# Kernel optimization log

Hardware: AMD Instinct MI355X
Metric: run time of the kernel (lower is better)

Reference implementation:

```python
import jax, jax.numpy as jnp
import numpy as np

NEG_SLOPE = 0.2  # PyG GATConv default


def add_self_loops(edge_index, num_nodes):
    loops = jnp.arange(num_nodes, dtype=edge_index.dtype)
    return jnp.concatenate([edge_index, jnp.stack([loops, loops])], axis=1)


def gat_conv(x, edge_index, W, att_src, att_dst, bias, heads, out_ch, concat):
    # x: [N, F_in]; edge_index: [2, E] with row0=src(j), row1=dst(i)
    N = x.shape[0]
    xl = (x @ W).reshape(N, heads, out_ch)              # [N, H, C]
    src, dst = edge_index[0], edge_index[1]
    a_src = jnp.einsum('nhc,hc->nh', xl, att_src)        # [N, H]
    a_dst = jnp.einsum('nhc,hc->nh', xl, att_dst)        # [N, H]
    alpha = jax.nn.leaky_relu(a_src[src] + a_dst[dst], NEG_SLOPE)  # [E, H]
    # segment softmax over incoming edges of each dst node
    m = jax.ops.segment_max(alpha, dst, num_segments=N)  # [N, H]
    e = jnp.exp(alpha - m[dst])
    denom = jax.ops.segment_sum(e, dst, num_segments=N)
    coef = e / (denom[dst] + 1e-16)                      # [E, H]
    msg = xl[src] * coef[..., None]                      # [E, H, C]
    out = jax.ops.segment_sum(msg, dst, num_segments=N)  # [N, H, C]
    out = out.reshape(N, heads * out_ch) if concat else out.mean(axis=1)
    return out + bias


def setup_inputs() -> dict:
    key = jax.random.key(0)
    ks = jax.random.split(key, 12)
    N, E = 50000, 800000
    nfeat, nhid, nheads, nclass = 512, 8, 8, 16
    hid = nhid * nheads  # 64
    s1 = 1.0 / np.sqrt(nfeat)
    s2 = 1.0 / np.sqrt(hid)
    return {
        'x': jax.random.normal(ks[0], (N, nfeat), jnp.float32),
        'edge_index': jax.random.randint(ks[1], (2, E), 0, N, jnp.int64 if jax.config.jax_enable_x64 else jnp.int32),
        'W1': jax.random.uniform(ks[2], (nfeat, hid), jnp.float32, -s1, s1),
        'att_src1': jax.random.uniform(ks[3], (nheads, nhid), jnp.float32, -s2, s2),
        'att_dst1': jax.random.uniform(ks[4], (nheads, nhid), jnp.float32, -s2, s2),
        'bias1': jnp.zeros((hid,), jnp.float32),
        'W2': jax.random.uniform(ks[5], (hid, nclass), jnp.float32, -s2, s2),
        'att_src2': jax.random.uniform(ks[6], (1, nclass), jnp.float32, -0.25, 0.25),
        'att_dst2': jax.random.uniform(ks[7], (1, nclass), jnp.float32, -0.25, 0.25),
        'bias2': jnp.zeros((nclass,), jnp.float32),
    }


def reference(x, edge_index, W1, att_src1, att_dst1, bias1, W2, att_src2, att_dst2, bias2):
    N = x.shape[0]
    ei = add_self_loops(edge_index, N)
    # dropout layers are identity at inference
    h = gat_conv(x, ei, W1, att_src1, att_dst1, bias1, heads=8, out_ch=8, concat=True)
    o = gat_conv(h, ei, W2, att_src2, att_dst2, bias2, heads=1, out_ch=16, concat=True)
    o = jax.nn.elu(o)
    return jax.nn.log_softmax(o, axis=1)
```

## Files before the change

### kernel.cpp

```cpp
#include <hip/hip_runtime.h>
#include <math.h>

#define NEG_SLOPE 0.2f

typedef short short8 __attribute__((ext_vector_type(8)));
typedef float floatx4 __attribute__((ext_vector_type(4)));

static __device__ __forceinline__ float bf2f(unsigned short u) {
  return __uint_as_float(((unsigned int)u) << 16);
}
static __device__ __forceinline__ unsigned short f2bf(float f) {
  unsigned int u = __float_as_uint(f);
  u = (u + 0x7fffu + ((u >> 16) & 1u)) >> 16;
  return (unsigned short)u;
}
static __device__ __forceinline__ unsigned int pack2(float a, float b) {
  return (unsigned int)f2bf(a) | ((unsigned int)f2bf(b) << 16);
}

__global__ void init_misc(const float* __restrict__ W1, unsigned short* __restrict__ W1t,
                          int* __restrict__ deg, int N) {
  int b = blockIdx.x;
  if (b < 128) {
    int i = b * 256 + threadIdx.x;
    int k = i >> 6, c = i & 63;
    W1t[c * 512 + k] = f2bf(W1[i]);
  } else {
    int n = (b - 128) * 256 + threadIdx.x;
    if (n < N) deg[n] = 1;
  }
}

__global__ __launch_bounds__(256) void gemm1_hist(const float* __restrict__ A,
                                                  const unsigned short* __restrict__ W1t,
                                                  const float* __restrict__ att_src,
                                                  const float* __restrict__ att_dst,
                                                  unsigned short* __restrict__ xlb,
                                                  float* __restrict__ a_src,
                                                  float* __restrict__ a_dst, int M,
                                                  const int* __restrict__ ei,
                                                  int* __restrict__ deg,
                                                  int* __restrict__ rank, int E,
                                                  int ipc, int G1) {
  __shared__ unsigned short As[64 * 72];
  __shared__ unsigned short Bs[64 * 72];
  if ((int)blockIdx.x >= G1) {
    int b = blockIdx.x - G1;
    int slice = b & 7;
    int chunk = b >> 3;
    int lo = (int)(((long long)slice * M) >> 3);
    int hi = (int)(((long long)(slice + 1) * M) >> 3);
    int beg = chunk * ipc;
    int end = min(beg + ipc, E);
    for (int i = beg + threadIdx.x; i < end; i += 256) {
      int d = ei[E + i];
      if (d >= lo && d < hi) rank[i] = atomicAdd(&deg[d], 1);
    }
    return;
  }
  int tid = threadIdx.x;
  int w = tid >> 6, lane = tid & 63;
  int q = lane >> 4, cl = lane & 15;
  int row0 = blockIdx.x << 6;
  floatx4 acc[4] = {};

  int sr = tid >> 2;
  int skq = (tid & 3) << 4;
  int arow = row0 + sr;
  bool okA = arow < M;
  const float* Aptr = A + (size_t)arow * 512 + skq;
  const unsigned short* Bptr = W1t + sr * 512 + skq;
  unsigned short* AsW = As + sr * 72 + skq;
  unsigned short* BsW = Bs + sr * 72 + skq;

  float4 ca0 = make_float4(0.f, 0.f, 0.f, 0.f), ca1 = ca0, ca2 = ca0, ca3 = ca0;
  uint4 cb0, cb1;
  if (okA) {
    ca0 = *(const float4*)(Aptr);
    ca1 = *(const float4*)(Aptr + 4);
    ca2 = *(const float4*)(Aptr + 8);
    ca3 = *(const float4*)(Aptr + 12);
  }
  cb0 = *(const uint4*)(Bptr);
  cb1 = *(const uint4*)(Bptr + 8);

#pragma unroll
  for (int k0 = 0; k0 < 512; k0 += 64) {
    __syncthreads();
    uint4 a0, a1;
    a0.x = pack2(ca0.x, ca0.y); a0.y = pack2(ca0.z, ca0.w);
    a0.z = pack2(ca1.x, ca1.y); a0.w = pack2(ca1.z, ca1.w);
    a1.x = pack2(ca2.x, ca2.y); a1.y = pack2(ca2.z, ca2.w);
    a1.z = pack2(ca3.x, ca3.y); a1.w = pack2(ca3.z, ca3.w);
    *(uint4*)(AsW) = a0;
    *(uint4*)(AsW + 8) = a1;
    *(uint4*)(BsW) = cb0;
    *(uint4*)(BsW + 8) = cb1;
    __syncthreads();
    if (k0 < 448) {
      ca0 = make_float4(0.f, 0.f, 0.f, 0.f); ca1 = ca0; ca2 = ca0; ca3 = ca0;
      if (okA) {
        ca0 = *(const float4*)(Aptr + k0 + 64);
        ca1 = *(const float4*)(Aptr + k0 + 68);
        ca2 = *(const float4*)(Aptr + k0 + 72);
        ca3 = *(const float4*)(Aptr + k0 + 76);
      }
      cb0 = *(const uint4*)(Bptr + k0 + 64);
      cb1 = *(const uint4*)(Bptr + k0 + 72);
    }
#pragma unroll
    for (int kk = 0; kk < 2; ++kk) {
      short8 af = *(const short8*)(As + (w * 16 + cl) * 72 + kk * 32 + q * 8);
#pragma unroll
      for (int t = 0; t < 4; ++t) {
        short8 bf = *(const short8*)(Bs + (t * 16 + cl) * 72 + kk * 32 + q * 8);
        acc[t] = __builtin_amdgcn_mfma_f32_16x16x32_bf16(af, bf, acc[t], 0, 0, 0);
      }
    }
  }

  float asv[4], adv[4];
#pragma unroll
  for (int t = 0; t < 4; ++t) {
    asv[t] = att_src[t * 16 + cl];
    adv[t] = att_dst[t * 16 + cl];
  }
#pragma unroll
  for (int reg = 0; reg < 4; ++reg) {
    int r = row0 + w * 16 + q * 4 + reg;
    bool ok = r < M;
#pragma unroll
    for (int t = 0; t < 4; ++t) {
      float v = acc[t][reg];
      if (ok) xlb[(size_t)r * 64 + t * 16 + cl] = f2bf(v);
      float ps = v * asv[t];
      float pd = v * adv[t];
      ps += __shfl_xor(ps, 1); pd += __shfl_xor(pd, 1);
      ps += __shfl_xor(ps, 2); pd += __shfl_xor(pd, 2);
      ps += __shfl_xor(ps, 4); pd += __shfl_xor(pd, 4);
      if (ok && (cl & 7) == 0) {
        int h = t * 2 + (cl >> 3);
        a_src[r * 8 + h] = ps;
        a_dst[r * 8 + h] = pd;
      }
    }
  }
}

__global__ __launch_bounds__(1024) void scan_single(const int* __restrict__ deg,
                                                    int* __restrict__ rowptr, int N) {
  __shared__ int wsum[16];
  int tid = threadIdx.x;
  int lane = tid & 63, wv = tid >> 6;
  int carry = 0;
  for (int base = 0; base < N; base += 8192) {
    int i0 = base + tid * 8;
    int d[8];
    if (i0 + 8 <= N) {
      int4 a = *(const int4*)(deg + i0);
      int4 b = *(const int4*)(deg + i0 + 4);
      d[0] = a.x; d[1] = a.y; d[2] = a.z; d[3] = a.w;
      d[4] = b.x; d[5] = b.y; d[6] = b.z; d[7] = b.w;
    } else {
#pragma unroll
      for (int k = 0; k < 8; ++k) d[k] = (i0 + k < N) ? deg[i0 + k] : 0;
    }
    int e[8];
    e[0] = d[0];
#pragma unroll
    for (int k = 1; k < 8; ++k) e[k] = e[k - 1] + d[k];
    int tot = e[7];
    int v = tot;
#pragma unroll
    for (int off = 1; off < 64; off <<= 1) {
      int t = __shfl_up(v, off, 64);
      if (lane >= off) v += t;
    }
    if (lane == 63) wsum[wv] = v;
    __syncthreads();
    int woff = carry;
    for (int w = 0; w < wv; ++w) woff += wsum[w];
    int excl = woff + v - tot;
    int r[8];
    r[0] = excl;
#pragma unroll
    for (int k = 1; k < 8; ++k) r[k] = excl + e[k - 1];
    if (i0 + 8 <= N) {
      *(int4*)(rowptr + i0)     = make_int4(r[0], r[1], r[2], r[3]);
      *(int4*)(rowptr + i0 + 4) = make_int4(r[4], r[5], r[6], r[7]);
    } else {
#pragma unroll
      for (int k = 0; k < 8; ++k)
        if (i0 + k < N) rowptr[i0 + k] = r[k];
    }
    int bt = 0;
#pragma unroll
    for (int w = 0; w < 16; ++w) bt += wsum[w];
    carry += bt;
    __syncthreads();
  }
  if (tid == 0) rowptr[N] = carry;
}

__global__ __launch_bounds__(256) void scatter_rank(const int* __restrict__ ei,
                                                    const int* __restrict__ rank,
                                                    const int* __restrict__ rowptr,
                                                    int* __restrict__ srcs,
                                                    int E, int N, int ipc) {
  int slice = blockIdx.x & 7;
  int chunk = blockIdx.x >> 3;
  int lo = (int)(((long long)slice * N) >> 3);
  int hi = (int)(((long long)(slice + 1) * N) >> 3);
  int total = E + N;
  int beg = chunk * ipc;
  int end = min(beg + ipc, total);
  for (int i = beg + threadIdx.x; i < end; i += 256) {
    int d = (i < E) ? ei[E + i] : (i - E);
    if (d >= lo && d < hi) {
      int pos = rowptr[d] + ((i < E) ? rank[i] : 0);
      srcs[pos] = (i < E) ? ei[i] : d;
    }
  }
}

__global__ __launch_bounds__(256) void agg1_fused(const int* __restrict__ rowptr,
                                                  const int* __restrict__ srcs,
                                                  const float* __restrict__ a_src,
                                                  const float* __restrict__ a_dst,
                                                  const unsigned short* __restrict__ xlb,
                                                  const float* __restrict__ bias1,
                                                  const float* __restrict__ W2,
                                                  const float* __restrict__ att_src2,
                                                  const float* __restrict__ att_dst2,
                                                  float* __restrict__ xl2,
                                                  float* __restrict__ a_src2,
                                                  float* __restrict__ a_dst2, int N) {
  __shared__ float W2s[64 * 16];
  __shared__ float hsm[4][64];
  int tid = threadIdx.x;
  W2s[tid]       = W2[tid];
  W2s[tid + 256] = W2[tid + 256];
  W2s[tid + 512] = W2[tid + 512];
  W2s[tid + 768] = W2[tid + 768];
  __syncthreads();

  int wv = tid >> 6, lane = tid & 63;
  int node = (blockIdx.x << 2) + wv;
  if (node >= N) return;
  int half = lane >> 5;
  int j = lane & 31;
  int h = j >> 2;
  int beg = rowptr[node], end = rowptr[node + 1];
  float ad = a_dst[node * 8 + h];
  float den = 0.f, acc0 = 0.f, acc1 = 0.f;

  int p = beg + half;
  bool v0 = p < end,      v1 = p + 2 < end,  v2 = p + 4 < end,  v3 = p + 6 < end;
  bool v4 = p + 8 < end,  v5 = p + 10 < end, v6 = p + 12 < end, v7 = p + 14 < end;
  int s0 = srcs[v0 ? p : beg];
  int s1 = srcs[v1 ? p + 2 : beg];
  int s2 = srcs[v2 ? p + 4 : beg];
  int s3 = srcs[v3 ? p + 6 : beg];
  int s4 = srcs[v4 ? p + 8 : beg];
  int s5 = srcs[v5 ? p + 10 : beg];
  int s6 = srcs[v6 ? p + 12 : beg];
  int s7 = srcs[v7 ? p + 14 : beg];
  while (v0) {
    int np = p + 16;
    bool u0 = np < end,      u1 = np + 2 < end,  u2 = np + 4 < end,  u3 = np + 6 < end;
    bool u4 = np + 8 < end,  u5 = np + 10 < end, u6 = np + 12 < end, u7 = np + 14 < end;
    int t0 = srcs[u0 ? np : beg];
    int t1 = srcs[u1 ? np + 2 : beg];
    int t2 = srcs[u2 ? np + 4 : beg];
    int t3 = srcs[u3 ? np + 6 : beg];
    int t4 = srcs[u4 ? np + 8 : beg];
    int t5 = srcs[u5 ? np + 10 : beg];
    int t6 = srcs[u6 ? np + 12 : beg];
    int t7 = srcs[u7 ? np + 14 : beg];
    float a0 = a_src[s0 * 8 + h] + ad;
    float a1 = a_src[s1 * 8 + h] + ad;
    float a2 = a_src[s2 * 8 + h] + ad;
    float a3 = a_src[s3 * 8 + h] + ad;
    float a4 = a_src[s4 * 8 + h] + ad;
    float a5 = a_src[s5 * 8 + h] + ad;
    float a6 = a_src[s6 * 8 + h] + ad;
    float a7 = a_src[s7 * 8 + h] + ad;
    ushort2 x0 = *(const ushort2*)(xlb + (size_t)s0 * 64 + 2 * j);
    ushort2 x1 = *(const ushort2*)(xlb + (size_t)s1 * 64 + 2 * j);
    ushort2 x2 = *(const ushort2*)(xlb + (size_t)s2 * 64 + 2 * j);
    ushort2 x3 = *(const ushort2*)(xlb + (size_t)s3 * 64 + 2 * j);
    ushort2 x4 = *(const ushort2*)(xlb + (size_t)s4 * 64 + 2 * j);
    ushort2 x5 = *(const ushort2*)(xlb + (size_t)s5 * 64 + 2 * j);
    ushort2 x6 = *(const ushort2*)(xlb + (size_t)s6 * 64 + 2 * j);
    ushort2 x7 = *(const ushort2*)(xlb + (size_t)s7 * 64 + 2 * j);
    a0 = a0 >= 0.f ? a0 : NEG_SLOPE * a0;
    a1 = a1 >= 0.f ? a1 : NEG_SLOPE * a1;
    a2 = a2 >= 0.f ? a2 : NEG_SLOPE * a2;
    a3 = a3 >= 0.f ? a3 : NEG_SLOPE * a3;
    a4 = a4 >= 0.f ? a4 : NEG_SLOPE * a4;
    a5 = a5 >= 0.f ? a5 : NEG_SLOPE * a5;
    a6 = a6 >= 0.f ? a6 : NEG_SLOPE * a6;
    a7 = a7 >= 0.f ? a7 : NEG_SLOPE * a7;
    float w0 = v0 ? __expf(a0) : 0.f;
    float w1 = v1 ? __expf(a1) : 0.f;
    float w2 = v2 ? __expf(a2) : 0.f;
    float w3 = v3 ? __expf(a3) : 0.f;
    float w4 = v4 ? __expf(a4) : 0.f;
    float w5 = v5 ? __expf(a5) : 0.f;
    float w6 = v6 ? __expf(a6) : 0.f;
    float w7 = v7 ? __expf(a7) : 0.f;
    den += ((w0 + w1) + (w2 + w3)) + ((w4 + w5) + (w6 + w7));
    acc0 += (w0 * bf2f(x0.x) + w1 * bf2f(x1.x)) + (w2 * bf2f(x2.x) + w3 * bf2f(x3.x)) +
            (w4 * bf2f(x4.x) + w5 * bf2f(x5.x)) + (w6 * bf2f(x6.x) + w7 * bf2f(x7.x));
    acc1 += (w0 * bf2f(x0.y) + w1 * bf2f(x1.y)) + (w2 * bf2f(x2.y) + w3 * bf2f(x3.y)) +
            (w4 * bf2f(x4.y) + w5 * bf2f(x5.y)) + (w6 * bf2f(x6.y) + w7 * bf2f(x7.y));
    p = np;
    s0 = t0; s1 = t1; s2 = t2; s3 = t3; s4 = t4; s5 = t5; s6 = t6; s7 = t7;
    v0 = u0; v1 = u1; v2 = u2; v3 = u3; v4 = u4; v5 = u5; v6 = u6; v7 = u7;
  }
  den  += __shfl_xor(den, 32);
  acc0 += __shfl_xor(acc0, 32);
  acc1 += __shfl_xor(acc1, 32);
  float inv = 1.f / (den + 1e-16f);
  float2 bv = *(const float2*)(bias1 + 2 * j);
  float h0 = acc0 * inv + bv.x;
  float h1 = acc1 * inv + bv.y;
  if (half == 0) {
    hsm[wv][2 * j]     = h0;
    hsm[wv][2 * j + 1] = h1;
  }
  if (lane < 16) {
    float sum = 0.f;
#pragma unroll
    for (int k = 0; k < 64; ++k) sum += hsm[wv][k] * W2s[k * 16 + lane];
    xl2[(size_t)node * 16 + lane] = sum;
    float ps = sum * att_src2[lane];
    float pd = sum * att_dst2[lane];
#pragma unroll
    for (int w = 8; w >= 1; w >>= 1) {
      ps += __shfl_xor(ps, w, 16);
      pd += __shfl_xor(pd, w, 16);
    }
    if (lane == 0) { a_src2[node] = ps; a_dst2[node] = pd; }
  }
}

__global__ __launch_bounds__(256) void agg2_fin(const int* __restrict__ rowptr,
                                                const int* __restrict__ srcs,
                                                const float* __restrict__ a_src2,
                                                const float* __restrict__ a_dst2,
                                                const float* __restrict__ xl2,
                                                const float* __restrict__ bias2,
                                                float* __restrict__ out, int N) {
  int t = blockIdx.x * blockDim.x + threadIdx.x;
  int node = t >> 4;
  int c = t & 15;
  if (node >= N) return;
  int beg = rowptr[node], end = rowptr[node + 1];
  float ad = a_dst2[node];
  float den = 0.f, acc = 0.f;
  int p = beg;
  bool v0 = true,          v1 = p + 1 < end, v2 = p + 2 < end, v3 = p + 3 < end;
  bool v4 = p + 4 < end,   v5 = p + 5 < end, v6 = p + 6 < end, v7 = p + 7 < end;
  int s0 = srcs[p];
  int s1 = srcs[v1 ? p + 1 : beg];
  int s2 = srcs[v2 ? p + 2 : beg];
  int s3 = srcs[v3 ? p + 3 : beg];
  int s4 = srcs[v4 ? p + 4 : beg];
  int s5 = srcs[v5 ? p + 5 : beg];
  int s6 = srcs[v6 ? p + 6 : beg];
  int s7 = srcs[v7 ? p + 7 : beg];
  while (v0) {
    int np = p + 8;
    bool u0 = np < end,     u1 = np + 1 < end, u2 = np + 2 < end, u3 = np + 3 < end;
    bool u4 = np + 4 < end, u5 = np + 5 < end, u6 = np + 6 < end, u7 = np + 7 < end;
    int t0 = srcs[u0 ? np : beg];
    int t1 = srcs[u1 ? np + 1 : beg];
    int t2 = srcs[u2 ? np + 2 : beg];
    int t3 = srcs[u3 ? np + 3 : beg];
    int t4 = srcs[u4 ? np + 4 : beg];
    int t5 = srcs[u5 ? np + 5 : beg];
    int t6 = srcs[u6 ? np + 6 : beg];
    int t7 = srcs[u7 ? np + 7 : beg];
    float a0 = a_src2[s0] + ad, a1 = a_src2[s1] + ad;
    float a2 = a_src2[s2] + ad, a3 = a_src2[s3] + ad;
    float a4 = a_src2[s4] + ad, a5 = a_src2[s5] + ad;
    float a6 = a_src2[s6] + ad, a7 = a_src2[s7] + ad;
    float x0 = xl2[(size_t)s0 * 16 + c], x1 = xl2[(size_t)s1 * 16 + c];
    float x2 = xl2[(size_t)s2 * 16 + c], x3 = xl2[(size_t)s3 * 16 + c];
    float x4 = xl2[(size_t)s4 * 16 + c], x5 = xl2[(size_t)s5 * 16 + c];
    float x6 = xl2[(size_t)s6 * 16 + c], x7 = xl2[(size_t)s7 * 16 + c];
    a0 = a0 >= 0.f ? a0 : NEG_SLOPE * a0;
    a1 = a1 >= 0.f ? a1 : NEG_SLOPE * a1;
    a2 = a2 >= 0.f ? a2 : NEG_SLOPE * a2;
    a3 = a3 >= 0.f ? a3 : NEG_SLOPE * a3;
    a4 = a4 >= 0.f ? a4 : NEG_SLOPE * a4;
    a5 = a5 >= 0.f ? a5 : NEG_SLOPE * a5;
    a6 = a6 >= 0.f ? a6 : NEG_SLOPE * a6;
    a7 = a7 >= 0.f ? a7 : NEG_SLOPE * a7;
    float w0 = v0 ? __expf(a0) : 0.f;
    float w1 = v1 ? __expf(a1) : 0.f;
    float w2 = v2 ? __expf(a2) : 0.f;
    float w3 = v3 ? __expf(a3) : 0.f;
    float w4 = v4 ? __expf(a4) : 0.f;
    float w5 = v5 ? __expf(a5) : 0.f;
    float w6 = v6 ? __expf(a6) : 0.f;
    float w7 = v7 ? __expf(a7) : 0.f;
    den += ((w0 + w1) + (w2 + w3)) + ((w4 + w5) + (w6 + w7));
    acc += (w0 * x0 + w1 * x1) + (w2 * x2 + w3 * x3) +
           (w4 * x4 + w5 * x5) + (w6 * x6 + w7 * x7);
    p = np;
    s0 = t0; s1 = t1; s2 = t2; s3 = t3; s4 = t4; s5 = t5; s6 = t6; s7 = t7;
    v0 = u0; v1 = u1; v2 = u2; v3 = u3; v4 = u4; v5 = u5; v6 = u6; v7 = u7;
  }
  float o = acc / (den + 1e-16f) + bias2[c];
  o = o > 0.f ? o : expm1f(o);
  float mx = o;
#pragma unroll
  for (int w = 8; w >= 1; w >>= 1) mx = fmaxf(mx, __shfl_xor(mx, w, 16));
  float e = __expf(o - mx);
  float ssum = e;
#pragma unroll
  for (int w = 8; w >= 1; w >>= 1) ssum += __shfl_xor(ssum, w, 16);
  out[(size_t)node * 16 + c] = o - mx - logf(ssum);
}

static inline size_t rnd16(size_t x) { return (x + 15) & ~(size_t)15; }

extern "C" void kernel_launch(void* const* d_in, const int* in_sizes, int n_in,
                              void* d_out, int out_size, void* d_ws, size_t ws_size,
                              hipStream_t stream) {
  const float* x        = (const float*)d_in[0];
  const int*   ei       = (const int*)d_in[1];
  const float* W1       = (const float*)d_in[2];
  const float* att_src1 = (const float*)d_in[3];
  const float* att_dst1 = (const float*)d_in[4];
  const float* bias1    = (const float*)d_in[5];
  const float* W2       = (const float*)d_in[6];
  const float* att_src2 = (const float*)d_in[7];
  const float* att_dst2 = (const float*)d_in[8];
  const float* bias2    = (const float*)d_in[9];
  float* out = (float*)d_out;

  int N = in_sizes[0] / 512;
  int E = in_sizes[1] / 2;

  char* ws = (char*)d_ws;
  unsigned short* xlb = (unsigned short*)ws;  ws += rnd16((size_t)N * 64 * 2);
  unsigned short* W1t = (unsigned short*)ws;  ws += rnd16((size_t)512 * 64 * 2);
  float* a_src1 = (float*)ws;                 ws += rnd16((size_t)N * 8 * 4);
  float* a_dst1 = (float*)ws;                 ws += rnd16((size_t)N * 8 * 4);
  float* xl2    = (float*)ws;                 ws += rnd16((size_t)N * 16 * 4);
  float* a_src2 = (float*)ws;                 ws += rnd16((size_t)N * 4);
  float* a_dst2 = (float*)ws;                 ws += rnd16((size_t)N * 4);
  int* deg      = (int*)ws;                   ws += rnd16((size_t)N * 4);
  int* rowptr   = (int*)ws;                   ws += rnd16((size_t)(N + 1) * 4);
  int* rank     = (int*)ws;                   ws += rnd16((size_t)E * 4);
  int* srcs     = (int*)ws;                   ws += rnd16((size_t)(E + N) * 4);

  const int NCHUNK = 256;
  int G1 = (N + 63) / 64;
  int ipc_h = (E + NCHUNK - 1) / NCHUNK;
  int ipc_s = (E + N + NCHUNK - 1) / NCHUNK;

  init_misc<<<128 + (N + 255) / 256, 256, 0, stream>>>(W1, W1t, deg, N);
  gemm1_hist<<<G1 + NCHUNK * 8, 256, 0, stream>>>(x, W1t, att_src1, att_dst1,
                                                  xlb, a_src1, a_dst1, N,
                                                  ei, deg, rank, E, ipc_h, G1);
  scan_single<<<1, 1024, 0, stream>>>(deg, rowptr, N);
  scatter_rank<<<NCHUNK * 8, 256, 0, stream>>>(ei, rank, rowptr, srcs, E, N, ipc_s);
  agg1_fused<<<(N + 3) / 4, 256, 0, stream>>>(rowptr, srcs, a_src1, a_dst1, xlb,
                                              bias1, W2, att_src2, att_dst2,
                                              xl2, a_src2, a_dst2, N);
  agg2_fin<<<((size_t)N * 16 + 255) / 256, 256, 0, stream>>>(rowptr, srcs, a_src2, a_dst2,
                                                             xl2, bias2, out, N);
}
```

Baseline: 296.3 us.

## Split x bf16 conversion into hist kernel and fuse degree scan into GEMM

```diff
diff --git a/kernel.cpp b/kernel.cpp
--- a/kernel.cpp
+++ b/kernel.cpp
@@ -13,9 +13,6 @@
   unsigned int u = __float_as_uint(f);
   u = (u + 0x7fffu + ((u >> 16) & 1u)) >> 16;
   return (unsigned short)u;
-}
-static __device__ __forceinline__ unsigned int pack2(float a, float b) {
-  return (unsigned int)f2bf(a) | ((unsigned int)f2bf(b) << 16);
 }
 
 __global__ void init_misc(const float* __restrict__ W1, unsigned short* __restrict__ W1t,
@@ -31,82 +28,144 @@
   }
 }
 
-__global__ __launch_bounds__(256) void gemm1_hist(const float* __restrict__ A,
+__global__ __launch_bounds__(256) void cvt_hist(const float* __restrict__ x,
+                                                unsigned short* __restrict__ xb,
+                                                const int* __restrict__ ei,
+                                                int* __restrict__ deg,
+                                                int* __restrict__ rank,
+                                                long long total, int E, int ipc, int NH) {
+  int b = blockIdx.x;
+  int tid = threadIdx.x;
+  if (b < NH) {
+    int beg = b * ipc;
+    int end = min(beg + ipc, E);
+    for (int i = beg + tid; i < end; i += 256) {
+      int d = ei[E + i];
+      rank[i] = atomicAdd(&deg[d], 1);
+    }
+    return;
+  }
+  long long base = (long long)(b - NH) * 2048;
+  long long i0 = base + tid * 4;
+  long long i1 = base + 1024 + tid * 4;
+  if (i1 + 4 <= total) {
+    float4 f0 = *(const float4*)(x + i0);
+    float4 f1 = *(const float4*)(x + i1);
+    ushort4 u0 = make_ushort4(f2bf(f0.x), f2bf(f0.y), f2bf(f0.z), f2bf(f0.w));
+    ushort4 u1 = make_ushort4(f2bf(f1.x), f2bf(f1.y), f2bf(f1.z), f2bf(f1.w));
+    *(ushort4*)(xb + i0) = u0;
+    *(ushort4*)(xb + i1) = u1;
+  } else {
+#pragma unroll
+    for (int k = 0; k < 4; ++k) {
+      if (i0 + k < total) xb[i0 + k] = f2bf(x[i0 + k]);
+      if (i1 + k < total) xb[i1 + k] = f2bf(x[i1 + k]);
+    }
+  }
+}
+
+__global__ __launch_bounds__(256) void gemm1_scan(const unsigned short* __restrict__ xb,
                                                   const unsigned short* __restrict__ W1t,
                                                   const float* __restrict__ att_src,
                                                   const float* __restrict__ att_dst,
                                                   unsigned short* __restrict__ xlb,
                                                   float* __restrict__ a_src,
                                                   float* __restrict__ a_dst, int M,
-                                                  const int* __restrict__ ei,
-                                                  int* __restrict__ deg,
-                                                  int* __restrict__ rank, int E,
-                                                  int ipc, int G1) {
+                                                  const int* __restrict__ deg,
+                                                  int* __restrict__ rowptr, int G1) {
   __shared__ unsigned short As[64 * 72];
   __shared__ unsigned short Bs[64 * 72];
+  int tid = threadIdx.x;
   if ((int)blockIdx.x >= G1) {
-    int b = blockIdx.x - G1;
-    int slice = b & 7;
-    int chunk = b >> 3;
-    int lo = (int)(((long long)slice * M) >> 3);
-    int hi = (int)(((long long)(slice + 1) * M) >> 3);
-    int beg = chunk * ipc;
-    int end = min(beg + ipc, E);
-    for (int i = beg + threadIdx.x; i < end; i += 256) {
-      int d = ei[E + i];
-      if (d >= lo && d < hi) rank[i] = atomicAdd(&deg[d], 1);
-    }
+    int* wsum = (int*)As;
+    int lane = tid & 63, wv = tid >> 6;
+    int carry = 0;
+    for (int base = 0; base < M; base += 2048) {
+      int i0 = base + tid * 8;
+      int d[8];
+      if (i0 + 8 <= M) {
+        int4 a = *(const int4*)(deg + i0);
+        int4 b = *(const int4*)(deg + i0 + 4);
+        d[0] = a.x; d[1] = a.y; d[2] = a.z; d[3] = a.w;
+        d[4] = b.x; d[5] = b.y; d[6] = b.z; d[7] = b.w;
+      } else {
+#pragma unroll
+        for (int k = 0; k < 8; ++k) d[k] = (i0 + k < M) ? deg[i0 + k] : 0;
+      }
+      int e[8];
+      e[0] = d[0];
+#pragma unroll
+      for (int k = 1; k < 8; ++k) e[k] = e[k - 1] + d[k];
+      int tot = e[7];
+      int v = tot;
+#pragma unroll
+      for (int off = 1; off < 64; off <<= 1) {
+        int t = __shfl_up(v, off, 64);
+        if (lane >= off) v += t;
+      }
+      if (lane == 63) wsum[wv] = v;
+      __syncthreads();
+      int woff = carry;
+      for (int w = 0; w < wv; ++w) woff += wsum[w];
+      int excl = woff + v - tot;
+      int r[8];
+      r[0] = excl;
+#pragma unroll
+      for (int k = 1; k < 8; ++k) r[k] = excl + e[k - 1];
+      if (i0 + 8 <= M) {
+        *(int4*)(rowptr + i0)     = make_int4(r[0], r[1], r[2], r[3]);
+        *(int4*)(rowptr + i0 + 4) = make_int4(r[4], r[5], r[6], r[7]);
+      } else {
+#pragma unroll
+        for (int k = 0; k < 8; ++k)
+          if (i0 + k < M) rowptr[i0 + k] = r[k];
+      }
+      int bt = (wsum[0] + wsum[1]) + (wsum[2] + wsum[3]);
+      __syncthreads();
+      carry += bt;
+    }
+    if (tid == 0) rowptr[M] = carry;
     return;
   }
-  int tid = threadIdx.x;
   int w = tid >> 6, lane = tid & 63;
   int q = lane >> 4, cl = lane & 15;
   int row0 = blockIdx.x << 6;
   floatx4 acc[4] = {};
 
   int sr = tid >> 2;
-  int skq = (tid & 3) << 4;
+  int c4 = tid & 3;
   int arow = row0 + sr;
   bool okA = arow < M;
-  const float* Aptr = A + (size_t)arow * 512 + skq;
-  const unsigned short* Bptr = W1t + sr * 512 + skq;
-  unsigned short* AsW = As + sr * 72 + skq;
-  unsigned short* BsW = Bs + sr * 72 + skq;
-
-  float4 ca0 = make_float4(0.f, 0.f, 0.f, 0.f), ca1 = ca0, ca2 = ca0, ca3 = ca0;
-  uint4 cb0, cb1;
+  const unsigned short* Ap = xb + (size_t)arow * 512;
+  const unsigned short* Bp = W1t + sr * 512;
+  unsigned short* AsW0 = As + sr * 72 + c4 * 8;
+  unsigned short* BsW0 = Bs + sr * 72 + c4 * 8;
+
+  uint4 a0 = make_uint4(0, 0, 0, 0), a1 = a0;
+  uint4 b0, b1;
   if (okA) {
-    ca0 = *(const float4*)(Aptr);
-    ca1 = *(const float4*)(Aptr + 4);
-    ca2 = *(const float4*)(Aptr + 8);
-    ca3 = *(const float4*)(Aptr + 12);
-  }
-  cb0 = *(const uint4*)(Bptr);
-  cb1 = *(const uint4*)(Bptr + 8);
+    a0 = *(const uint4*)(Ap + c4 * 8);
+    a1 = *(const uint4*)(Ap + 32 + c4 * 8);
+  }
+  b0 = *(const uint4*)(Bp + c4 * 8);
+  b1 = *(const uint4*)(Bp + 32 + c4 * 8);
 
 #pragma unroll
   for (int k0 = 0; k0 < 512; k0 += 64) {
     __syncthreads();
-    uint4 a0, a1;
-    a0.x = pack2(ca0.x, ca0.y); a0.y = pack2(ca0.z, ca0.w);
-    a0.z = pack2(ca1.x, ca1.y); a0.w = pack2(ca1.z, ca1.w);
-    a1.x = pack2(ca2.x, ca2.y); a1.y = pack2(ca2.z, ca2.w);
-    a1.z = pack2(ca3.x, ca3.y); a1.w = pack2(ca3.z, ca3.w);
-    *(uint4*)(AsW) = a0;
-    *(uint4*)(AsW + 8) = a1;
-    *(uint4*)(BsW) = cb0;
-    *(uint4*)(BsW + 8) = cb1;
+    *(uint4*)(AsW0)      = a0;
+    *(uint4*)(AsW0 + 32) = a1;
+    *(uint4*)(BsW0)      = b0;
+    *(uint4*)(BsW0 + 32) = b1;
     __syncthreads();
     if (k0 < 448) {
-      ca0 = make_float4(0.f, 0.f, 0.f, 0.f); ca1 = ca0; ca2 = ca0; ca3 = ca0;
+      a0 = make_uint4(0, 0, 0, 0); a1 = a0;
       if (okA) {
-        ca0 = *(const float4*)(Aptr + k0 + 64);
-        ca1 = *(const float4*)(Aptr + k0 + 68);
-        ca2 = *(const float4*)(Aptr + k0 + 72);
-        ca3 = *(const float4*)(Aptr + k0 + 76);
-      }
-      cb0 = *(const uint4*)(Bptr + k0 + 64);
-      cb1 = *(const uint4*)(Bptr + k0 + 72);
+        a0 = *(const uint4*)(Ap + k0 + 64 + c4 * 8);
+        a1 = *(const uint4*)(Ap + k0 + 96 + c4 * 8);
+      }
+      b0 = *(const uint4*)(Bp + k0 + 64 + c4 * 8);
+      b1 = *(const uint4*)(Bp + k0 + 96 + c4 * 8);
     }
 #pragma unroll
     for (int kk = 0; kk < 2; ++kk) {
@@ -145,61 +204,6 @@
       }
     }
   }
-}
-
-__global__ __launch_bounds__(1024) void scan_single(const int* __restrict__ deg,
-                                                    int* __restrict__ rowptr, int N) {
-  __shared__ int wsum[16];
-  int tid = threadIdx.x;
-  int lane = tid & 63, wv = tid >> 6;
-  int carry = 0;
-  for (int base = 0; base < N; base += 8192) {
-    int i0 = base + tid * 8;
-    int d[8];
-    if (i0 + 8 <= N) {
-      int4 a = *(const int4*)(deg + i0);
-      int4 b = *(const int4*)(deg + i0 + 4);
-      d[0] = a.x; d[1] = a.y; d[2] = a.z; d[3] = a.w;
-      d[4] = b.x; d[5] = b.y; d[6] = b.z; d[7] = b.w;
-    } else {
-#pragma unroll
-      for (int k = 0; k < 8; ++k) d[k] = (i0 + k < N) ? deg[i0 + k] : 0;
-    }
-    int e[8];
-    e[0] = d[0];
-#pragma unroll
-    for (int k = 1; k < 8; ++k) e[k] = e[k - 1] + d[k];
-    int tot = e[7];
-    int v = tot;
-#pragma unroll
-    for (int off = 1; off < 64; off <<= 1) {
-      int t = __shfl_up(v, off, 64);
-      if (lane >= off) v += t;
-    }
-    if (lane == 63) wsum[wv] = v;
-    __syncthreads();
-    int woff = carry;
-    for (int w = 0; w < wv; ++w) woff += wsum[w];
-    int excl = woff + v - tot;
-    int r[8];
-    r[0] = excl;
-#pragma unroll
-    for (int k = 1; k < 8; ++k) r[k] = excl + e[k - 1];
-    if (i0 + 8 <= N) {
-      *(int4*)(rowptr + i0)     = make_int4(r[0], r[1], r[2], r[3]);
-      *(int4*)(rowptr + i0 + 4) = make_int4(r[4], r[5], r[6], r[7]);
-    } else {
-#pragma unroll
-      for (int k = 0; k < 8; ++k)
-        if (i0 + k < N) rowptr[i0 + k] = r[k];
-    }
-    int bt = 0;
-#pragma unroll
-    for (int w = 0; w < 16; ++w) bt += wsum[w];
-    carry += bt;
-    __syncthreads();
-  }
-  if (tid == 0) rowptr[N] = carry;
 }
 
 __global__ __launch_bounds__(256) void scatter_rank(const int* __restrict__ ei,
@@ -446,6 +450,7 @@
   int E = in_sizes[1] / 2;
 
   char* ws = (char*)d_ws;
+  unsigned short* xb  = (unsigned short*)ws;  ws += rnd16((size_t)N * 512 * 2);
   unsigned short* xlb = (unsigned short*)ws;  ws += rnd16((size_t)N * 64 * 2);
   unsigned short* W1t = (unsigned short*)ws;  ws += rnd16((size_t)512 * 64 * 2);
   float* a_src1 = (float*)ws;                 ws += rnd16((size_t)N * 8 * 4);
@@ -459,15 +464,17 @@
   int* srcs     = (int*)ws;                   ws += rnd16((size_t)(E + N) * 4);
 
   const int NCHUNK = 256;
+  const int NH = 256;
+  long long total = (long long)N * 512;
+  int GC = (int)((total + 2047) / 2048);
   int G1 = (N + 63) / 64;
-  int ipc_h = (E + NCHUNK - 1) / NCHUNK;
+  int ipc_h = (E + NH - 1) / NH;
   int ipc_s = (E + N + NCHUNK - 1) / NCHUNK;
 
   init_misc<<<128 + (N + 255) / 256, 256, 0, stream>>>(W1, W1t, deg, N);
-  gemm1_hist<<<G1 + NCHUNK * 8, 256, 0, stream>>>(x, W1t, att_src1, att_dst1,
-                                                  xlb, a_src1, a_dst1, N,
-                                                  ei, deg, rank, E, ipc_h, G1);
-  scan_single<<<1, 1024, 0, stream>>>(deg, rowptr, N);
+  cvt_hist<<<NH + GC, 256, 0, stream>>>(x, xb, ei, deg, rank, total, E, ipc_h, NH);
+  gemm1_scan<<<G1 + 1, 256, 0, stream>>>(xb, W1t, att_src1, att_dst1,
+                                         xlb, a_src1, a_dst1, N, deg, rowptr, G1);
   scatter_rank<<<NCHUNK * 8, 256, 0, stream>>>(ei, rank, rowptr, srcs, E, N, ipc_s);
   agg1_fused<<<(N + 3) / 4, 256, 0, stream>>>(rowptr, srcs, a_src1, a_dst1, xlb,
                                               bias1, W2, att_src2, att_dst2,
```

Result: faster. 283.5 us (-4.3%).
